# Optimization experiments

Measured on AMD Instinct MI355X. Metric: run time of the kernel, lower is better.

## Reference

```python
import jax, jax.numpy as jnp
import numpy as np


def _cayley_table(p=4, q=1):
    """Dense geometric-product table C[a,b,c] for Cl(p,q): e_a * e_b = sum_c C[a,b,c] e_c.
    Basis blades indexed by bitmask over n = p+q generators; metric diag(+1*p, -1*q)."""
    n = p + q
    dim = 1 << n  # 32 for Cl(4,1)
    metric = [1.0] * p + [-1.0] * q
    C = np.zeros((dim, dim, dim), dtype=np.float32)
    for a in range(dim):
        for b in range(dim):
            # sign from reordering generators into canonical order
            s = 1.0
            t = a >> 1
            while t:
                if bin(t & b).count('1') & 1:
                    s = -s
                t >>= 1
            # metric contraction of repeated generators
            common = a & b
            for i in range(n):
                if (common >> i) & 1:
                    s *= metric[i]
            C[a, b, a ^ b] += s
    return C

CAYLEY = jnp.asarray(_cayley_table())  # [32, 32, 32]
EPS = 1e-6


def reference(x, W_in, b_in, w_h, w_x, W_out, b_out):
    B, S, N, D = x.shape
    H, M = w_h.shape[0], w_h.shape[2]  # hidden_channels=16, d_mv=32
    x_flat = x.reshape(B, S, N * D)

    # Pre-contract weights with the Cayley table once (outside the scan):
    # geometric_linear_layer(h, w)[b,o,k] = sum_{i,m,n} h[b,i,m] w[o,i,n] C[m,n,k]
    Wh = jnp.einsum('oin,mnk->imok', w_h, CAYLEY).reshape(H * M, H * M)
    Wx = jnp.einsum('oin,mnk->imok', w_x, CAYLEY).reshape(H * M, H * M)

    h0 = jnp.zeros((B, H * M), x.dtype)

    def step(h, x_t):  # h: [B, H*M], x_t: [B, N*D]
        x_emb = x_t @ W_in + b_in                      # [B, H*M]
        delta = h @ Wh + x_emb @ Wx                    # geometric linear layers
        h_new = h + delta                              # residual update
        # manifold normalization: unit L2 norm per multivector channel
        hv = h_new.reshape(B, H, M)
        norm = jnp.linalg.norm(hv, axis=-1, keepdims=True)
        hv = hv / (norm + EPS)
        h_new = hv.reshape(B, H * M)
        out = x_t + h_new @ W_out + b_out              # residual output
        return h_new, out

    _, outs = jax.lax.scan(step, h0, jnp.swapaxes(x_flat, 0, 1))  # [S, B, N*D]
    return jnp.swapaxes(outs, 0, 1).reshape(B, S, N, D)


def setup_inputs() -> dict:
    key = jax.random.key(0)
    ks = jax.random.split(key, 5)
    B, S, N, D = 256, 1024, 5, 6
    H, M = 16, 32
    x = jax.random.normal(ks[0], (B, S, N, D), dtype=jnp.float32)
    W_in = jax.random.normal(ks[1], (N * D, H * M), dtype=jnp.float32) / np.sqrt(N * D)
    b_in = jnp.zeros((H * M,), dtype=jnp.float32)
    w_h = jax.random.normal(ks[2], (H, H, M), dtype=jnp.float32) * 0.01
    w_x = jax.random.normal(ks[3], (H, H, M), dtype=jnp.float32) * 0.01
    W_out = jax.random.normal(ks[4], (H * M, N * D), dtype=jnp.float32) / np.sqrt(H * M)
    b_out = jnp.zeros((N * D,), dtype=jnp.float32)
    return {"x": x, "W_in": W_in, "b_in": b_in, "w_h": w_h, "w_x": w_x, "W_out": W_out, "b_out": b_out}
```

## Files before the change

### kernel.cpp

```cpp
#include <hip/hip_runtime.h>

#define S_   1024
#define ND   30
#define EPS_ 1e-6f

typedef __attribute__((ext_vector_type(8))) short bf16x8;
typedef __attribute__((ext_vector_type(4))) float f32x4;
typedef __attribute__((ext_vector_type(2))) _Float16 h2;
typedef __attribute__((ext_vector_type(8))) _Float16 h8;

__device__ __forceinline__ int cayley_neg(int a, int b) {
    int par = 0;
    for (int t = a >> 1; t; t >>= 1) par ^= __popc(t & b) & 1;
    par ^= ((a & b) >> 4) & 1;
    return par & 1;
}

__device__ __forceinline__ void split2(float v, ushort& hi, ushort& lo) {
    unsigned bv = __float_as_uint(v);
    hi = (ushort)(bv >> 16);
    float hv = __uint_as_float(bv & 0xffff0000u);
    lo = (ushort)(__float_as_uint(v - hv) >> 16);
}

__device__ __forceinline__ ushort f2h(float v) {
    _Float16 h = (_Float16)v;
    ushort u;
    __builtin_memcpy(&u, &h, 2);
    return u;
}

__device__ __forceinline__ float dpp_xor1(float v) {
    return __int_as_float(__builtin_amdgcn_update_dpp(
        0, __float_as_int(v), 0xB1 , 0xF, 0xF, true));
}
__device__ __forceinline__ float dpp_xor2(float v) {
    return __int_as_float(__builtin_amdgcn_update_dpp(
        0, __float_as_int(v), 0x4E , 0xF, 0xF, true));
}

#define BAR() asm volatile("s_waitcnt lgkmcnt(0)\n\ts_barrier" ::: "memory")

__launch_bounds__(512, 2)
__global__ void versor_kernel(const float* __restrict__ x,
                              const float* __restrict__ W_in,
                              const float* __restrict__ b_in,
                              const float* __restrict__ w_h,
                              const float* __restrict__ w_x,
                              const float* __restrict__ W_out,
                              const float* __restrict__ b_out,
                              float* __restrict__ out) {
    const int b   = blockIdx.x;
    const int tid = threadIdx.x;
    const int w   = tid >> 6;
    const int ln  = tid & 63;
    const int g   = ln >> 4;
    const int cl  = ln & 15;
    const int op  = ln >> 5;
    const int oo  = 2 * w + op;
    const int kk  = ln & 31;
    const int oc  = tid >> 5;
    const int lc  = tid & 31;

    __shared__ ushort ghi[2][1024];
    __shared__ ushort glo[2][1024];
    __shared__ __align__(16) ushort hf[2][512];
    __shared__ float red[2][512];

    bf16x8 bh[2][2], bl[2][2];
    #pragma unroll
    for (int opi = 0; opi < 2; ++opi) {
        #pragma unroll
        for (int nt = 0; nt < 2; ++nt) {
            const int o = 2 * w + opi;
            const int n = nt * 16 + cl;
            #pragma unroll
            for (int j = 0; j < 8; ++j) {
                const int k = g * 8 + j;
                float wv = (k < 16) ? w_h[(o * 16 + k) * 32 + n]
                                    : w_x[(o * 16 + (k - 16)) * 32 + n];
                ushort h_, l_; split2(wv, h_, l_);
                bh[opi][nt][j] = (short)h_;
                bl[opi][nt][j] = (short)l_;
            }
        }
    }

    float win_reg[ND];
    #pragma unroll
    for (int p = 0; p < ND; ++p) win_reg[p] = W_in[p * 512 + tid];
    const float bin_reg = b_in[tid];

    const int pc = (lc < ND) ? lc : 0;
    h2 wout_h2[16];
    #pragma unroll
    for (int j = 0; j < 16; ++j) {
        wout_h2[j][0] = (_Float16)W_out[(oc * 32 + 2 * j) * ND + pc];
        wout_h2[j][1] = (_Float16)W_out[(oc * 32 + 2 * j + 1) * ND + pc];
    }
    const float bout_reg = (tid < ND) ? b_out[tid] : 0.0f;

    float sgn[16];
    for (int mt = 0; mt < 2; ++mt)
        for (int nt = 0; nt < 2; ++nt)
            for (int r = 0; r < 4; ++r) {
                int m = mt * 16 + g * 4 + r;
                int n = nt * 16 + cl;
                sgn[mt * 8 + nt * 4 + r] = cayley_neg(m, n) ? -1.0f : 1.0f;
            }

    const int eh = (kk >> 4) * 512 + (oo >> 3) * 128 + (kk & 15) * 8 + (oo & 7);
    const int ex = (lc >> 4) * 512 + (2 + (oc >> 3)) * 128 + (lc & 15) * 8 + (oc & 7);
    const int ea = g * 128 + cl * 8;

    const int l_src = (g << 4) | (cl ^ ((g & 1) << 2) ^ ((g >> 1) << 3));

    ghi[0][eh] = 0; glo[0][eh] = 0;

    float h_reg = 0.0f, xv_prev = 0.0f;
    const float* xrow = x   + (size_t)b * S_ * ND;
    float*       orow = out + (size_t)b * S_ * ND;
    const f32x4 z4 = {0.f, 0.f, 0.f, 0.f};

    for (int s = 0; s <= S_; ++s) {
        const int p = s & 1;

        float xv_cur = 0.0f;
        if (s < S_) {
            const float* xp = xrow + s * ND;
            xv_cur = (tid < ND) ? xp[tid] : 0.0f;
            float xe0 = bin_reg, xe1 = 0.f, xe2 = 0.f, xe3 = 0.f;
            #pragma unroll
            for (int q = 0; q < 28; q += 4) {
                xe0 = fmaf(xp[q + 0], win_reg[q + 0], xe0);
                xe1 = fmaf(xp[q + 1], win_reg[q + 1], xe1);
                xe2 = fmaf(xp[q + 2], win_reg[q + 2], xe2);
                xe3 = fmaf(xp[q + 3], win_reg[q + 3], xe3);
            }
            xe0 = fmaf(xp[28], win_reg[28], xe0);
            xe1 = fmaf(xp[29], win_reg[29], xe1);
            float xe = (xe0 + xe1) + (xe2 + xe3);
            ushort xh, xl; split2(xe, xh, xl);
            ghi[p][ex] = xh; glo[p][ex] = xl;
        }

        if (s > 0) {
            const ushort* hp = &hf[p][oc * 32];
            float oa0 = 0.0f, oa1 = 0.0f;
            #pragma unroll
            for (int qq = 0; qq < 2; ++qq) {
                h8 hv0 = *(const h8*)(hp + qq * 8);
                h8 hv1 = *(const h8*)(hp + 16 + qq * 8);
                #pragma unroll
                for (int jj = 0; jj < 4; ++jj) {
                    h2 a0 = {hv0[2 * jj], hv0[2 * jj + 1]};
                    h2 a1 = {hv1[2 * jj], hv1[2 * jj + 1]};
                    oa0 = __builtin_amdgcn_fdot2(a0, wout_h2[qq * 4 + jj], oa0, false);
                    oa1 = __builtin_amdgcn_fdot2(a1, wout_h2[8 + qq * 4 + jj], oa1, false);
                }
            }
            red[p][oc * 32 + lc] = oa0 + oa1;
        }

        BAR();

        if (s > 0 && tid < ND) {
            float s0 = 0.f, s1 = 0.f, s2 = 0.f, s3 = 0.f;
            #pragma unroll
            for (int jg = 0; jg < 16; jg += 4) {
                s0 += red[p][(jg + 0) * 32 + tid];
                s1 += red[p][(jg + 1) * 32 + tid];
                s2 += red[p][(jg + 2) * 32 + tid];
                s3 += red[p][(jg + 3) * 32 + tid];
            }
            float ov = xv_prev + bout_reg + ((s0 + s1) + (s2 + s3));
            orow[(size_t)(s - 1) * ND + tid] = ov;
        }

        if (s < S_) {
            bf16x8 ah0 = *(const bf16x8*)&ghi[p][ea];
            bf16x8 ah1 = *(const bf16x8*)&ghi[p][ea + 512];
            bf16x8 al0 = *(const bf16x8*)&glo[p][ea];
            bf16x8 al1 = *(const bf16x8*)&glo[p][ea + 512];

            f32x4 acc[2][2][2];
            #pragma unroll
            for (int opi = 0; opi < 2; ++opi) {
                #pragma unroll
                for (int nt = 0; nt < 2; ++nt) {
                    f32x4 t = __builtin_amdgcn_mfma_f32_16x16x32_bf16(al0, bl[opi][nt], z4, 0, 0, 0);
                    t = __builtin_amdgcn_mfma_f32_16x16x32_bf16(ah0, bl[opi][nt], t, 0, 0, 0);
                    t = __builtin_amdgcn_mfma_f32_16x16x32_bf16(al0, bh[opi][nt], t, 0, 0, 0);
                    acc[opi][0][nt] = __builtin_amdgcn_mfma_f32_16x16x32_bf16(ah0, bh[opi][nt], t, 0, 0, 0);
                    f32x4 u = __builtin_amdgcn_mfma_f32_16x16x32_bf16(al1, bl[opi][nt], z4, 0, 0, 0);
                    u = __builtin_amdgcn_mfma_f32_16x16x32_bf16(ah1, bl[opi][nt], u, 0, 0, 0);
                    u = __builtin_amdgcn_mfma_f32_16x16x32_bf16(al1, bh[opi][nt], u, 0, 0, 0);
                    acc[opi][1][nt] = __builtin_amdgcn_mfma_f32_16x16x32_bf16(ah1, bh[opi][nt], u, 0, 0, 0);
                }
            }

            float Y[2][2][4];
            #pragma unroll
            for (int opi = 0; opi < 2; ++opi)
                #pragma unroll
                for (int nt = 0; nt < 2; ++nt)
                    #pragma unroll
                    for (int r = 0; r < 4; ++r)
                        Y[opi][nt][r] = fmaf(sgn[nt * 4 + r],
                                             acc[opi][0][nt][r],
                                             sgn[8 + (nt ^ 1) * 4 + r] * acc[opi][1][nt ^ 1][r]);
            float Z[2][2];
            #pragma unroll
            for (int opi = 0; opi < 2; ++opi) {
                #pragma unroll
                for (int kt = 0; kt < 2; ++kt) {
                    float ya0 = Y[opi][kt][0] + dpp_xor1(Y[opi][kt][1]);
                    float ya2 = Y[opi][kt][2] + dpp_xor1(Y[opi][kt][3]);
                    float z = ya0 + dpp_xor2(ya2);
                    z += __shfl_xor(z, 20, 64);
                    z += __shfl_xor(z, 40, 64);
                    Z[opi][kt] = z;
                }
            }
            float za  = (g & 2) ? Z[1][0] : Z[0][0];
            float zb  = (g & 2) ? Z[1][1] : Z[0][1];
            float sel = (g & 1) ? zb : za;
            const float delta = __shfl(sel, l_src, 64);

            float hc = h_reg + delta;
            float ss = hc * hc;
            ss += dpp_xor1(ss);
            ss += dpp_xor2(ss);
            ss += __shfl_xor(ss, 4, 32);
            ss += __shfl_xor(ss, 8, 32);
            ss += __shfl_xor(ss, 16, 32);
            h_reg = hc / (sqrtf(ss) + EPS_);

            ushort hh, hl; split2(h_reg, hh, hl);
            ghi[p ^ 1][eh] = hh; glo[p ^ 1][eh] = hl;
            hf[p ^ 1][oo * 32 + kk] = f2h(h_reg);
        }

        xv_prev = xv_cur;
    }
}

extern "C" void kernel_launch(void* const* d_in, const int* in_sizes, int n_in,
                              void* d_out, int out_size, void* d_ws, size_t ws_size,
                              hipStream_t stream) {
    const float* x     = (const float*)d_in[0];
    const float* W_in  = (const float*)d_in[1];
    const float* b_in  = (const float*)d_in[2];
    const float* w_h   = (const float*)d_in[3];
    const float* w_x   = (const float*)d_in[4];
    const float* W_out = (const float*)d_in[5];
    const float* b_out = (const float*)d_in[6];
    float* outp = (float*)d_out;

    versor_kernel<<<256, 512, 0, stream>>>(x, W_in, b_in, w_h, w_x, W_out, b_out, outp);
}
```

Measured before the change: 1.394 ms.

## Prefetch x rows two steps ahead into LDS and compute next-step embedding early

Instead of every thread reading all 30 x values of the current timestep from global memory on the critical path, 30 threads prefetch the row two steps ahead into a register and stage it into a small double-buffered LDS array. The input embedding for step s+1 is computed from LDS with vector loads during step s and written into the other ghi/glo buffer. This takes the global-load latency out of the serial recurrence, at the cost of extra LDS traffic and a dependency on existing barriers for the xt buffer ordering.

```diff
diff --git a/kernel.cpp b/kernel.cpp
--- a/kernel.cpp
+++ b/kernel.cpp
@@ -66,6 +66,7 @@
     __shared__ ushort glo[2][1024];
     __shared__ __align__(16) ushort hf[2][512];
     __shared__ float red[2][512];
+    __shared__ __align__(16) float xt[2][32];
 
     bf16x8 bh[2][2], bl[2][2];
     #pragma unroll
@@ -115,33 +116,41 @@
 
     const int l_src = (g << 4) | (cl ^ ((g & 1) << 2) ^ ((g >> 1) << 3));
 
-    ghi[0][eh] = 0; glo[0][eh] = 0;
-
-    float h_reg = 0.0f, xv_prev = 0.0f;
     const float* xrow = x   + (size_t)b * S_ * ND;
     float*       orow = out + (size_t)b * S_ * ND;
     const f32x4 z4 = {0.f, 0.f, 0.f, 0.f};
 
+    ghi[0][eh] = 0; glo[0][eh] = 0;
+    {
+        const float* xp = xrow;
+        float xe0 = bin_reg, xe1 = 0.f, xe2 = 0.f, xe3 = 0.f;
+        #pragma unroll
+        for (int q = 0; q < 28; q += 4) {
+            xe0 = fmaf(xp[q + 0], win_reg[q + 0], xe0);
+            xe1 = fmaf(xp[q + 1], win_reg[q + 1], xe1);
+            xe2 = fmaf(xp[q + 2], win_reg[q + 2], xe2);
+            xe3 = fmaf(xp[q + 3], win_reg[q + 3], xe3);
+        }
+        xe0 = fmaf(xp[28], win_reg[28], xe0);
+        xe1 = fmaf(xp[29], win_reg[29], xe1);
+        float xe = (xe0 + xe1) + (xe2 + xe3);
+        ushort xh, xl; split2(xe, xh, xl);
+        ghi[0][ex] = xh; glo[0][ex] = xl;
+    }
+    float xreg = 0.0f;
+    if (tid < ND) xreg = xrow[1 * ND + tid];
+
+    float h_reg = 0.0f, xv_prev = 0.0f;
+
     for (int s = 0; s <= S_; ++s) {
         const int p = s & 1;
 
         float xv_cur = 0.0f;
-        if (s < S_) {
-            const float* xp = xrow + s * ND;
-            xv_cur = (tid < ND) ? xp[tid] : 0.0f;
-            float xe0 = bin_reg, xe1 = 0.f, xe2 = 0.f, xe3 = 0.f;
-            #pragma unroll
-            for (int q = 0; q < 28; q += 4) {
-                xe0 = fmaf(xp[q + 0], win_reg[q + 0], xe0);
-                xe1 = fmaf(xp[q + 1], win_reg[q + 1], xe1);
-                xe2 = fmaf(xp[q + 2], win_reg[q + 2], xe2);
-                xe3 = fmaf(xp[q + 3], win_reg[q + 3], xe3);
-            }
-            xe0 = fmaf(xp[28], win_reg[28], xe0);
-            xe1 = fmaf(xp[29], win_reg[29], xe1);
-            float xe = (xe0 + xe1) + (xe2 + xe3);
-            ushort xh, xl; split2(xe, xh, xl);
-            ghi[p][ex] = xh; glo[p][ex] = xl;
+        if (s < S_) xv_cur = (tid < ND) ? xrow[(size_t)s * ND + tid] : 0.0f;
+        if (tid < ND) {
+            xt[(s + 1) & 1][tid] = xreg;
+            int nr = (s + 2 < S_) ? s + 2 : S_ - 1;
+            xreg = xrow[(size_t)nr * ND + tid];
         }
 
         if (s > 0) {
@@ -175,6 +184,24 @@
             }
             float ov = xv_prev + bout_reg + ((s0 + s1) + (s2 + s3));
             orow[(size_t)(s - 1) * ND + tid] = ov;
+        }
+
+        if (s + 1 < S_) {
+            const float* xq = &xt[(s + 1) & 1][0];
+            float xe0 = bin_reg, xe1 = 0.f, xe2 = 0.f, xe3 = 0.f;
+            #pragma unroll
+            for (int q = 0; q < 28; q += 4) {
+                float4 x4 = *(const float4*)(xq + q);
+                xe0 = fmaf(x4.x, win_reg[q + 0], xe0);
+                xe1 = fmaf(x4.y, win_reg[q + 1], xe1);
+                xe2 = fmaf(x4.z, win_reg[q + 2], xe2);
+                xe3 = fmaf(x4.w, win_reg[q + 3], xe3);
+            }
+            xe0 = fmaf(xq[28], win_reg[28], xe0);
+            xe1 = fmaf(xq[29], win_reg[29], xe1);
+            float xe = (xe0 + xe1) + (xe2 + xe3);
+            ushort xh, xl; split2(xe, xh, xl);
+            ghi[p ^ 1][ex] = xh; glo[p ^ 1][ex] = xl;
         }
 
         if (s < S_) {
```

New measurement: 1.616 ms. +15.9%, slower.
